# Optimization experiments

Hardware: AMD Instinct MI355X
Metric: run time of the kernel (lower is better)

The kernel has to match this reference:

```python
import jax, jax.numpy as jnp
import numpy as np

N_NODES = 40000
N_EDGES = 640000
N_GRAPHS = 64
D_IN = 128
HID = 200
OUT = 2


def _lin(key, fin, fout):
    # torch nn.Linear-style init: U(-1/sqrt(fin), 1/sqrt(fin))
    kw, kb = jax.random.split(key)
    s = 1.0 / np.sqrt(fin)
    W = jax.random.uniform(kw, (fin, fout), jnp.float32, -s, s)
    b = jax.random.uniform(kb, (fout,), jnp.float32, -s, s)
    return W, b


def setup_inputs() -> dict:
    key = jax.random.key(0)
    ks = jax.random.split(key, 10)
    x = jax.random.normal(ks[0], (N_NODES, D_IN), jnp.float32)
    edge_index = jax.random.randint(ks[1], (2, N_EDGES), 0, N_NODES, jnp.int32)
    batch = jnp.sort(jax.random.randint(ks[2], (N_NODES,), 0, N_GRAPHS, jnp.int32))
    W1, b1 = _lin(ks[3], D_IN, HID)
    W2, b2 = _lin(ks[4], HID, HID)
    W3, b3 = _lin(ks[5], HID, HID)
    Wg, bg = _lin(ks[6], HID, HID)
    Wc1, bc1 = _lin(ks[7], HID, HID // 2)
    Wc2, bc2 = _lin(ks[8], HID // 2, OUT)
    return {"x": x, "edge_index": edge_index, "batch": batch,
            "W1": W1, "b1": b1, "W2": W2, "b2": b2, "W3": W3, "b3": b3,
            "Wg": Wg, "bg": bg, "Wc1": Wc1, "bc1": bc1, "Wc2": Wc2, "bc2": bc2}


def reference(x, edge_index, batch, W1, b1, W2, b2, W3, b3, Wg, bg, Wc1, bc1, Wc2, bc2):
    n = x.shape[0]
    # GCNConv with self-loops + symmetric normalization (PyG defaults)
    loop = jnp.arange(n, dtype=edge_index.dtype)
    src = jnp.concatenate([edge_index[0], loop])  # [E+N]
    dst = jnp.concatenate([edge_index[1], loop])
    deg = jax.ops.segment_sum(jnp.ones(src.shape, x.dtype), dst, num_segments=n)
    dinv = jax.lax.rsqrt(jnp.maximum(deg, 1.0))  # deg >= 1 with self-loops
    norm = (dinv[src] * dinv[dst])[:, None]      # [E+N, 1]

    def gcn(h, W, b):
        m = (h @ W)[src] * norm                  # gather + scale per edge
        return jax.ops.segment_sum(m, dst, num_segments=n) + b

    h = jax.nn.relu(gcn(x, W1, b1))
    h = jax.nn.relu(gcn(h, W2, b2))
    h = jax.nn.relu(gcn(h, W3, b3))

    gate = jax.nn.sigmoid(h @ Wg + bg)
    hg = h * gate

    # global_mean_pool over batch assignment
    sums = jax.ops.segment_sum(hg, batch, num_segments=N_GRAPHS)
    cnt = jax.ops.segment_sum(jnp.ones((n,), x.dtype), batch, num_segments=N_GRAPHS)
    pooled = sums / jnp.maximum(cnt, 1.0)[:, None]

    # classifier (dropout is identity in eval)
    hidden = jax.nn.relu(pooled @ Wc1 + bc1)
    logits = hidden @ Wc2 + bc2                  # [N_GRAPHS, 2]
    return logits
```

## Files before the change

kernel.cpp:

```cpp
#include <hip/hip_runtime.h>

#define NG 64
#define HIDW 200
#define DIN 128
#define KPAD 224
#define POOL_NC 8

typedef _Float16 half4_t __attribute__((ext_vector_type(4)));
typedef _Float16 half8_t __attribute__((ext_vector_type(8)));
typedef float floatx4 __attribute__((ext_vector_type(4)));


__global__ void build_kernel(const int* __restrict__ dst, int* __restrict__ counts,
                             const int* __restrict__ batch, int* __restrict__ gs,
                             int E, int n) {
  int i = blockIdx.x * 256 + threadIdx.x;
  if (i < E) atomicAdd(&counts[dst[i]], 1);
  if (i < n) {
    int b = batch[i];
    if (i == 0) {
      for (int g = 0; g <= b; ++g) gs[g] = 0;
    } else {
      int bp = batch[i - 1];
      for (int g = bp + 1; g <= b; ++g) gs[g] = i;
    }
    if (i == n - 1) {
      for (int g = b + 1; g <= NG; ++g) gs[g] = n;
    }
  }
}


__global__ __launch_bounds__(256) void scan1_kernel(const int* __restrict__ counts,
                                                    int* __restrict__ blocksum,
                                                    float* __restrict__ dinv, int n) {
  __shared__ int s[256];
  int tid = threadIdx.x;
  int i = blockIdx.x * 256 + tid;
  int c = (i < n) ? counts[i] : 0;
  if (i < n) dinv[i] = rsqrtf((float)(c + 1));
  s[tid] = c;
  __syncthreads();
#pragma unroll
  for (int off = 128; off > 0; off >>= 1) {
    if (tid < off) s[tid] += s[tid + off];
    __syncthreads();
  }
  if (tid == 0) blocksum[blockIdx.x] = s[0];
}

__global__ __launch_bounds__(1024) void scan2_kernel(int* __restrict__ blocksum, int nb) {
  __shared__ int s[1024];
  int tid = threadIdx.x;
  int v = (tid < nb) ? blocksum[tid] : 0;
  s[tid] = v;
  __syncthreads();
  for (int off = 1; off < 1024; off <<= 1) {
    int t = (tid >= off) ? s[tid - off] : 0;
    __syncthreads();
    s[tid] += t;
    __syncthreads();
  }
  if (tid < nb) blocksum[tid] = s[tid] - v;
}

__global__ __launch_bounds__(256) void scan3_kernel(const int* __restrict__ counts,
                                                    const int* __restrict__ blocksum,
                                                    int* __restrict__ row_ptr, int n) {
  __shared__ int s[256];
  int tid = threadIdx.x;
  int i = blockIdx.x * 256 + tid;
  int c = (i < n) ? counts[i] : 0;
  s[tid] = c;
  __syncthreads();
  for (int off = 1; off < 256; off <<= 1) {
    int t = (tid >= off) ? s[tid - off] : 0;
    __syncthreads();
    s[tid] += t;
    __syncthreads();
  }
  int base = blocksum[blockIdx.x];
  if (i < n) row_ptr[i] = base + s[tid] - c;
  if (i == n - 1) row_ptr[n] = base + s[tid];
}

__global__ void fill_kernel(const int* __restrict__ src, const int* __restrict__ dst,
                            const int* __restrict__ row_ptr, int* __restrict__ fill,
                            int* __restrict__ csr_src, int E) {
  int e = blockIdx.x * 256 + threadIdx.x;
  if (e >= E) return;
  int d = dst[e];
  int pos = row_ptr[d] + atomicAdd(&fill[d], 1);
  csr_src[pos] = src[e];
}


__global__ void wprep_kernel(const float* __restrict__ W1, const float* __restrict__ W2,
                             const float* __restrict__ W3, const float* __restrict__ Wg,
                             _Float16* __restrict__ o1h, _Float16* __restrict__ o1l,
                             _Float16* __restrict__ o2h, _Float16* __restrict__ o2l,
                             _Float16* __restrict__ o3h, _Float16* __restrict__ o3l,
                             _Float16* __restrict__ ogh, _Float16* __restrict__ ogl) {
  int wsel = blockIdx.y;
  const float* W = (wsel == 0) ? W1 : (wsel == 1) ? W2 : (wsel == 2) ? W3 : Wg;
  _Float16* WTh = (wsel == 0) ? o1h : (wsel == 1) ? o2h : (wsel == 2) ? o3h : ogh;
  _Float16* WTl = (wsel == 0) ? o1l : (wsel == 1) ? o2l : (wsel == 2) ? o3l : ogl;
  int K  = (wsel == 0) ? DIN : HIDW;
  int KP = (wsel == 0) ? DIN : KPAD;
  int idx = blockIdx.x * 256 + threadIdx.x;
  if (idx >= 256 * KP) return;
  int col = idx / KP, k = idx % KP;
  float v = (col < HIDW && k < K) ? W[(long)k * HIDW + col] : 0.f;
  _Float16 h = (_Float16)v;
  WTh[idx] = h;
  WTl[idx] = (_Float16)(v - (float)h);
}


__global__ void cvt_kernel(const float* __restrict__ x, const float* __restrict__ dinv,
                           _Float16* __restrict__ g0, int n) {
  int t = blockIdx.x * 256 + threadIdx.x;
  if (t >= n * 32) return;
  int node = t >> 5, q = t & 31;
  float di = dinv[node];
  float4 v = *(const float4*)&x[(long)node * 128 + q * 4];
  half4_t r = {(_Float16)(di * v.x), (_Float16)(di * v.y),
               (_Float16)(di * v.z), (_Float16)(di * v.w)};
  ((half4_t*)g0)[(long)node * 32 + q] = r;
}


template <int C>
__global__ __launch_bounds__(256) void agg_kernel(const _Float16* __restrict__ g,
                                                  const int* __restrict__ row_ptr,
                                                  const int* __restrict__ csr_src,
                                                  const float* __restrict__ dinv,
                                                  _Float16* __restrict__ out, int n) {
  int node = blockIdx.x * 4 + (threadIdx.x >> 6);
  int lane = threadIdx.x & 63;
  if (node >= n || lane >= C) return;
  const half4_t* __restrict__ hp = (const half4_t*)g;
  int e0 = row_ptr[node], e1 = row_ptr[node + 1];
  half4_t self = hp[(long)node * C + lane];
  float ax = (float)self.x, ay = (float)self.y;
  float az = (float)self.z, aw = (float)self.w;

  int e = e0;
  for (; e + 16 <= e1; e += 16) {
    int sI[16];
#pragma unroll
    for (int j = 0; j < 16; ++j) sI[j] = csr_src[e + j];
    half4_t vv[16];
#pragma unroll
    for (int j = 0; j < 16; ++j) vv[j] = hp[(long)sI[j] * C + lane];
#pragma unroll
    for (int j = 0; j < 16; ++j) {
      ax += (float)vv[j].x; ay += (float)vv[j].y;
      az += (float)vv[j].z; aw += (float)vv[j].w;
    }
  }
  if (e + 8 <= e1) {
    int sI[8];
#pragma unroll
    for (int j = 0; j < 8; ++j) sI[j] = csr_src[e + j];
    half4_t vv[8];
#pragma unroll
    for (int j = 0; j < 8; ++j) vv[j] = hp[(long)sI[j] * C + lane];
#pragma unroll
    for (int j = 0; j < 8; ++j) {
      ax += (float)vv[j].x; ay += (float)vv[j].y;
      az += (float)vv[j].z; aw += (float)vv[j].w;
    }
    e += 8;
  }
  if (e + 4 <= e1) {
    int sI[4];
#pragma unroll
    for (int j = 0; j < 4; ++j) sI[j] = csr_src[e + j];
    half4_t vv[4];
#pragma unroll
    for (int j = 0; j < 4; ++j) vv[j] = hp[(long)sI[j] * C + lane];
#pragma unroll
    for (int j = 0; j < 4; ++j) {
      ax += (float)vv[j].x; ay += (float)vv[j].y;
      az += (float)vv[j].z; aw += (float)vv[j].w;
    }
    e += 4;
  }
  for (; e < e1; ++e) {
    int s = csr_src[e];
    half4_t v = hp[(long)s * C + lane];
    ax += (float)v.x; ay += (float)v.y; az += (float)v.z; aw += (float)v.w;
  }
  float di = dinv[node];
  half4_t r = {(_Float16)(di * ax), (_Float16)(di * ay),
               (_Float16)(di * az), (_Float16)(di * aw)};
  ((half4_t*)out)[(long)node * C + lane] = r;
}


template <int KP, int MODE, int DSCALE>
__global__ __launch_bounds__(256, 2) void mgemm_kernel(const _Float16* __restrict__ A,
                                                       const _Float16* __restrict__ WTh,
                                                       const _Float16* __restrict__ WTl,
                                                       const float* __restrict__ bias,
                                                       const float* __restrict__ dinv,
                                                       _Float16* __restrict__ out, int N) {
  constexpr int LDK = KP + 8;
  __shared__ _Float16 Bh[64][LDK];
  __shared__ _Float16 Bl[64][LDK];
  int tid = threadIdx.x;
  int b = blockIdx.x;
  int strip = (b >> 3) & 3;
  int rg = (b & 7) + 8 * (b >> 5);
  int col0 = strip * 64;

  {
    int c = tid >> 2;
    int ks = (tid & 3) * (KP / 4);
    const _Float16* gh = WTh + (long)(col0 + c) * KP + ks;
    const _Float16* gl = WTl + (long)(col0 + c) * KP + ks;
#pragma unroll
    for (int j = 0; j < KP / 32; ++j) {
      *(half8_t*)&Bh[c][ks + j * 8] = *(const half8_t*)(gh + j * 8);
      *(half8_t*)&Bl[c][ks + j * 8] = *(const half8_t*)(gl + j * 8);
    }
  }
  __syncthreads();

  int lane = tid & 63;
  int wid = tid >> 6;
  int row0 = rg * 256 + wid * 64;
  if (row0 >= N) return;
  int l15 = lane & 15;
  int lq = lane >> 4;

  const _Float16* __restrict__ pa = A + (long)(row0 + l15) * KP + lq * 8;

  floatx4 acc[4][4];
#pragma unroll
  for (int i = 0; i < 4; ++i)
#pragma unroll
    for (int j = 0; j < 4; ++j) acc[i][j] = (floatx4){0.f, 0.f, 0.f, 0.f};

#pragma unroll
  for (int k0 = 0; k0 < KP; k0 += 32) {
    half8_t a[4];
#pragma unroll
    for (int rf = 0; rf < 4; ++rf)
      a[rf] = *(const half8_t*)(pa + (long)rf * 16 * KP + k0);
#pragma unroll
    for (int cf = 0; cf < 4; ++cf) {
      half8_t bh = *(const half8_t*)&Bh[cf * 16 + l15][k0 + lq * 8];
#pragma unroll
      for (int rf = 0; rf < 4; ++rf)
        acc[rf][cf] = __builtin_amdgcn_mfma_f32_16x16x32_f16(a[rf], bh, acc[rf][cf], 0, 0, 0);
    }
#pragma unroll
    for (int cf = 0; cf < 4; ++cf) {
      half8_t bl = *(const half8_t*)&Bl[cf * 16 + l15][k0 + lq * 8];
#pragma unroll
      for (int rf = 0; rf < 4; ++rf)
        acc[rf][cf] = __builtin_amdgcn_mfma_f32_16x16x32_f16(a[rf], bl, acc[rf][cf], 0, 0, 0);
    }
  }

#pragma unroll
  for (int cf = 0; cf < 4; ++cf) {
    int col = col0 + cf * 16 + l15;
    if (col >= KPAD) continue;
    float bs = (col < HIDW) ? bias[col] : 0.f;
#pragma unroll
    for (int rf = 0; rf < 4; ++rf) {
      int rbase = row0 + rf * 16 + lq * 4;
#pragma unroll
      for (int j = 0; j < 4; ++j) {
        int row = rbase + j;
        float v = acc[rf][cf][j] + bs;
        if (MODE == 1) v = fmaxf(v, 0.f);
        if (MODE == 2) {
          float hv = (float)A[(long)row * KP + col];
          v = hv * (1.f / (1.f + __expf(-v)));
        }
        if (DSCALE) v *= dinv[row];
        if (col >= HIDW) v = 0.f;
        out[(long)row * KPAD + col] = (_Float16)v;
      }
    }
  }
}


__global__ __launch_bounds__(256) void pool_partial_kernel(const _Float16* __restrict__ gated,
                                                           const int* __restrict__ gs,
                                                           float* __restrict__ partial, int n) {
  int g = blockIdx.x;
  int c = blockIdx.y;
  int f = threadIdx.x;
  int s = gs[g], e = gs[g + 1];
  int len = e - s;
  int chunk = (len + POOL_NC - 1) / POOL_NC;
  int i0 = s + c * chunk;
  int i1 = i0 + chunk; if (i1 > e) i1 = e;
  if (f < HIDW) {
    float acc = 0.f;
    for (int i = i0; i < i1; ++i) acc += (float)gated[(long)i * KPAD + f];
    partial[(g * POOL_NC + c) * HIDW + f] = acc;
  }
}


__global__ void classifier_kernel(const float* __restrict__ partial,
                                  const int* __restrict__ gs,
                                  const float* __restrict__ Wc1, const float* __restrict__ bc1,
                                  const float* __restrict__ Wc2, const float* __restrict__ bc2,
                                  float* __restrict__ out) {
  int g = blockIdx.x;
  int tid = threadIdx.x;
  __shared__ float pg[HIDW];
  __shared__ float hid[100];
  if (tid < HIDW) {
    float acc = 0.f;
#pragma unroll
    for (int c = 0; c < POOL_NC; ++c) acc += partial[(g * POOL_NC + c) * HIDW + tid];
    float cnt = fmaxf((float)(gs[g + 1] - gs[g]), 1.f);
    pg[tid] = acc / cnt;
  }
  __syncthreads();
  if (tid < 100) {
    float a = bc1[tid];
    for (int k = 0; k < HIDW; ++k) a = fmaf(pg[k], Wc1[k * 100 + tid], a);
    hid[tid] = fmaxf(a, 0.f);
  }
  __syncthreads();
  if (tid < 2) {
    float a = bc2[tid];
    for (int k = 0; k < 100; ++k) a = fmaf(hid[k], Wc2[k * 2 + tid], a);
    out[g * 2 + tid] = a;
  }
}


extern "C" void kernel_launch(void* const* d_in, const int* in_sizes, int n_in,
                              void* d_out, int out_size, void* d_ws, size_t ws_size,
                              hipStream_t stream) {
  const float* x    = (const float*)d_in[0];
  const int*   ei   = (const int*)d_in[1];
  const int*   batch= (const int*)d_in[2];
  const float* W1 = (const float*)d_in[3];  const float* b1 = (const float*)d_in[4];
  const float* W2 = (const float*)d_in[5];  const float* b2 = (const float*)d_in[6];
  const float* W3 = (const float*)d_in[7];  const float* b3 = (const float*)d_in[8];
  const float* Wg = (const float*)d_in[9];  const float* bg = (const float*)d_in[10];
  const float* Wc1= (const float*)d_in[11]; const float* bc1= (const float*)d_in[12];
  const float* Wc2= (const float*)d_in[13]; const float* bc2= (const float*)d_in[14];
  float* out = (float*)d_out;

  const int n = in_sizes[0] / DIN;
  const int E = in_sizes[1] / 2;
  const int* src = ei;
  const int* dst = ei + E;
  const int nb256 = (n + 255) / 256;

  int* counts   = (int*)d_ws;
  int* fill     = counts + n;
  int* row_ptr  = fill + n;
  int* gs       = row_ptr + (n + 4);
  int* blocksum = gs + 68;
  float* dinv   = (float*)(blocksum + 1024);
  int* csr_src  = (int*)(dinv + n);
  float* partial= (float*)(csr_src + E);
  _Float16* wt1h = (_Float16*)(partial + NG * POOL_NC * HIDW);
  _Float16* wt1l = wt1h + 256 * 128;
  _Float16* wt2h = wt1l + 256 * 128;
  _Float16* wt2l = wt2h + 256 * KPAD;
  _Float16* wt3h = wt2l + 256 * KPAD;
  _Float16* wt3l = wt3h + 256 * KPAD;
  _Float16* wtgh = wt3l + 256 * KPAD;
  _Float16* wtgl = wtgh + 256 * KPAD;
  _Float16* xh   = wtgl + 256 * KPAD;
  _Float16* bufA = xh + (long)n * DIN;
  _Float16* bufB = bufA + (long)n * KPAD;

  hipMemsetAsync(counts, 0, (size_t)2 * n * sizeof(int), stream);

  dim3 wgrid((256 * KPAD + 255) / 256, 4);
  wprep_kernel<<<wgrid, 256, 0, stream>>>(W1, W2, W3, Wg, wt1h, wt1l, wt2h, wt2l,
                                          wt3h, wt3l, wtgh, wtgl);

  int eb = (E + 255) / 256;
  build_kernel<<<eb, 256, 0, stream>>>(dst, counts, batch, gs, E, n);
  scan1_kernel<<<nb256, 256, 0, stream>>>(counts, blocksum, dinv, n);
  cvt_kernel<<<(n * 32 + 255) / 256, 256, 0, stream>>>(x, dinv, xh, n);
  scan2_kernel<<<1, 1024, 0, stream>>>(blocksum, nb256);
  scan3_kernel<<<nb256, 256, 0, stream>>>(counts, blocksum, row_ptr, n);
  fill_kernel<<<eb, 256, 0, stream>>>(src, dst, row_ptr, fill, csr_src, E);

  int ab = (n + 3) / 4;
  int gb = ((nb256 + 7) / 8) * 8 * 4;

  agg_kernel<32><<<ab, 256, 0, stream>>>(xh, row_ptr, csr_src, dinv, bufA, n);
  mgemm_kernel<DIN, 1, 1><<<gb, 256, 0, stream>>>(bufA, wt1h, wt1l, b1, dinv, bufB, n);
  agg_kernel<56><<<ab, 256, 0, stream>>>(bufB, row_ptr, csr_src, dinv, bufA, n);
  mgemm_kernel<KPAD, 1, 1><<<gb, 256, 0, stream>>>(bufA, wt2h, wt2l, b2, dinv, bufB, n);
  agg_kernel<56><<<ab, 256, 0, stream>>>(bufB, row_ptr, csr_src, dinv, bufA, n);
  mgemm_kernel<KPAD, 1, 0><<<gb, 256, 0, stream>>>(bufA, wt3h, wt3l, b3, dinv, bufB, n);
  mgemm_kernel<KPAD, 2, 0><<<gb, 256, 0, stream>>>(bufB, wtgh, wtgl, bg, dinv, bufA, n);
  dim3 pgrid(NG, POOL_NC);
  pool_partial_kernel<<<pgrid, 256, 0, stream>>>(bufA, gs, partial, n);
  classifier_kernel<<<NG, 256, 0, stream>>>(partial, gs, Wc1, bc1, Wc2, bc2, out);
}
```

Baseline: 329.7 us.

## Store node features in 32-column slices for cache-local gather aggregation

Feature buffers change from row-major [node][K] to a sliced layout [K/32][node][32]. Aggregation blocks now each handle one 64-byte slice, so a block's random gathers all fall in one slice array that fits better in cache, and the output uses nontemporal stores. The GEMM, conversion and pooling kernels are rewritten to read and write the sliced layout. In exchange, each aggregation wave now uses only 8 of its 64 lanes, and the GEMM A loads and output stores use a different stride pattern.

```diff
diff --git a/kernel.cpp b/kernel.cpp
--- a/kernel.cpp
+++ b/kernel.cpp
@@ -126,22 +126,33 @@
   float4 v = *(const float4*)&x[(long)node * 128 + q * 4];
   half4_t r = {(_Float16)(di * v.x), (_Float16)(di * v.y),
                (_Float16)(di * v.z), (_Float16)(di * v.w)};
-  ((half4_t*)g0)[(long)node * 32 + q] = r;
-}
-
-
-template <int C>
+  ((half4_t*)g0)[((long)(q >> 3) * n + node) * 8 + (q & 7)] = r;
+}
+
+
+template <int NSLICE>
 __global__ __launch_bounds__(256) void agg_kernel(const _Float16* __restrict__ g,
                                                   const int* __restrict__ row_ptr,
                                                   const int* __restrict__ csr_src,
                                                   const float* __restrict__ dinv,
                                                   _Float16* __restrict__ out, int n) {
-  int node = blockIdx.x * 4 + (threadIdx.x >> 6);
+  int slot = blockIdx.x & 7;
+  int nb = blockIdx.x >> 3;
   int lane = threadIdx.x & 63;
-  if (node >= n || lane >= C) return;
-  const half4_t* __restrict__ hp = (const half4_t*)g;
+  int wv = threadIdx.x >> 6;
+  int slice, node;
+  if (NSLICE == 7) {
+    if (slot == 7) return;
+    slice = slot;
+    node = nb * 4 + wv;
+  } else {
+    slice = slot >> 1;
+    node = (nb * 2 + (slot & 1)) * 4 + wv;
+  }
+  if (node >= n || lane >= 8) return;
+  const half4_t* __restrict__ hp = (const half4_t*)g + (long)slice * n * 8;
   int e0 = row_ptr[node], e1 = row_ptr[node + 1];
-  half4_t self = hp[(long)node * C + lane];
+  half4_t self = hp[(long)node * 8 + lane];
   float ax = (float)self.x, ay = (float)self.y;
   float az = (float)self.z, aw = (float)self.w;
 
@@ -152,7 +163,7 @@
     for (int j = 0; j < 16; ++j) sI[j] = csr_src[e + j];
     half4_t vv[16];
 #pragma unroll
-    for (int j = 0; j < 16; ++j) vv[j] = hp[(long)sI[j] * C + lane];
+    for (int j = 0; j < 16; ++j) vv[j] = hp[(long)sI[j] * 8 + lane];
 #pragma unroll
     for (int j = 0; j < 16; ++j) {
       ax += (float)vv[j].x; ay += (float)vv[j].y;
@@ -165,7 +176,7 @@
     for (int j = 0; j < 8; ++j) sI[j] = csr_src[e + j];
     half4_t vv[8];
 #pragma unroll
-    for (int j = 0; j < 8; ++j) vv[j] = hp[(long)sI[j] * C + lane];
+    for (int j = 0; j < 8; ++j) vv[j] = hp[(long)sI[j] * 8 + lane];
 #pragma unroll
     for (int j = 0; j < 8; ++j) {
       ax += (float)vv[j].x; ay += (float)vv[j].y;
@@ -179,7 +190,7 @@
     for (int j = 0; j < 4; ++j) sI[j] = csr_src[e + j];
     half4_t vv[4];
 #pragma unroll
-    for (int j = 0; j < 4; ++j) vv[j] = hp[(long)sI[j] * C + lane];
+    for (int j = 0; j < 4; ++j) vv[j] = hp[(long)sI[j] * 8 + lane];
 #pragma unroll
     for (int j = 0; j < 4; ++j) {
       ax += (float)vv[j].x; ay += (float)vv[j].y;
@@ -189,13 +200,13 @@
   }
   for (; e < e1; ++e) {
     int s = csr_src[e];
-    half4_t v = hp[(long)s * C + lane];
+    half4_t v = hp[(long)s * 8 + lane];
     ax += (float)v.x; ay += (float)v.y; az += (float)v.z; aw += (float)v.w;
   }
   float di = dinv[node];
   half4_t r = {(_Float16)(di * ax), (_Float16)(di * ay),
                (_Float16)(di * az), (_Float16)(di * aw)};
-  ((half4_t*)out)[(long)node * C + lane] = r;
+  __builtin_nontemporal_store(r, (half4_t*)out + (long)slice * n * 8 + (long)node * 8 + lane);
 }
 
 
@@ -235,8 +246,6 @@
   int l15 = lane & 15;
   int lq = lane >> 4;
 
-  const _Float16* __restrict__ pa = A + (long)(row0 + l15) * KP + lq * 8;
-
   floatx4 acc[4][4];
 #pragma unroll
   for (int i = 0; i < 4; ++i)
@@ -245,10 +254,11 @@
 
 #pragma unroll
   for (int k0 = 0; k0 < KP; k0 += 32) {
+    const _Float16* as = A + ((long)(k0 >> 5) * N + row0 + l15) * 32 + lq * 8;
     half8_t a[4];
 #pragma unroll
     for (int rf = 0; rf < 4; ++rf)
-      a[rf] = *(const half8_t*)(pa + (long)rf * 16 * KP + k0);
+      a[rf] = *(const half8_t*)(as + rf * 16 * 32);
 #pragma unroll
     for (int cf = 0; cf < 4; ++cf) {
       half8_t bh = *(const half8_t*)&Bh[cf * 16 + l15][k0 + lq * 8];
@@ -270,6 +280,7 @@
     int col = col0 + cf * 16 + l15;
     if (col >= KPAD) continue;
     float bs = (col < HIDW) ? bias[col] : 0.f;
+    long obase = ((long)(col >> 5) * N) * 32 + (col & 31);
 #pragma unroll
     for (int rf = 0; rf < 4; ++rf) {
       int rbase = row0 + rf * 16 + lq * 4;
@@ -279,12 +290,12 @@
         float v = acc[rf][cf][j] + bs;
         if (MODE == 1) v = fmaxf(v, 0.f);
         if (MODE == 2) {
-          float hv = (float)A[(long)row * KP + col];
+          float hv = (float)A[((long)(col >> 5) * N + row) * 32 + (col & 31)];
           v = hv * (1.f / (1.f + __expf(-v)));
         }
         if (DSCALE) v *= dinv[row];
         if (col >= HIDW) v = 0.f;
-        out[(long)row * KPAD + col] = (_Float16)v;
+        out[obase + (long)row * 32] = (_Float16)v;
       }
     }
   }
@@ -303,8 +314,9 @@
   int i0 = s + c * chunk;
   int i1 = i0 + chunk; if (i1 > e) i1 = e;
   if (f < HIDW) {
+    const _Float16* p = gated + ((long)(f >> 5) * n) * 32 + (f & 31);
     float acc = 0.f;
-    for (int i = i0; i < i1; ++i) acc += (float)gated[(long)i * KPAD + f];
+    for (int i = i0; i < i1; ++i) acc += (float)p[(long)i * 32];
     partial[(g * POOL_NC + c) * HIDW + f] = acc;
   }
 }
@@ -395,14 +407,15 @@
   scan3_kernel<<<nb256, 256, 0, stream>>>(counts, blocksum, row_ptr, n);
   fill_kernel<<<eb, 256, 0, stream>>>(src, dst, row_ptr, fill, csr_src, E);
 
-  int ab = (n + 3) / 4;
+  int ag7 = 8 * ((n + 3) / 4);
+  int ag4 = 8 * ((n + 7) / 8);
   int gb = ((nb256 + 7) / 8) * 8 * 4;
 
-  agg_kernel<32><<<ab, 256, 0, stream>>>(xh, row_ptr, csr_src, dinv, bufA, n);
+  agg_kernel<4><<<ag4, 256, 0, stream>>>(xh, row_ptr, csr_src, dinv, bufA, n);
   mgemm_kernel<DIN, 1, 1><<<gb, 256, 0, stream>>>(bufA, wt1h, wt1l, b1, dinv, bufB, n);
-  agg_kernel<56><<<ab, 256, 0, stream>>>(bufB, row_ptr, csr_src, dinv, bufA, n);
+  agg_kernel<7><<<ag7, 256, 0, stream>>>(bufB, row_ptr, csr_src, dinv, bufA, n);
   mgemm_kernel<KPAD, 1, 1><<<gb, 256, 0, stream>>>(bufA, wt2h, wt2l, b2, dinv, bufB, n);
-  agg_kernel<56><<<ab, 256, 0, stream>>>(bufB, row_ptr, csr_src, dinv, bufA, n);
+  agg_kernel<7><<<ag7, 256, 0, stream>>>(bufB, row_ptr, csr_src, dinv, bufA, n);
   mgemm_kernel<KPAD, 1, 0><<<gb, 256, 0, stream>>>(bufA, wt3h, wt3l, b3, dinv, bufB, n);
   mgemm_kernel<KPAD, 2, 0><<<gb, 256, 0, stream>>>(bufB, wtgh, wtgl, bg, dinv, bufA, n);
   dim3 pgrid(NG, POOL_NC);
```

Result: slower. 769.8 us (+133.5%).
